# Kernel optimization log

Hardware: AMD Instinct MI355X
Metric: run time of the kernel (lower is better)

The kernel has to match this reference:

```python
import jax, jax.numpy as jnp
import numpy as np

B, N, C = 4, 100000, 64
S = 256            # img_size
RADIUS_PX = 1.5    # radius in pixels
K = 8              # points_per_pixel
GAMMA = 1.0
R_NDC = RADIUS_PX / S * 2.0  # radius in NDC, as in forward()


def setup_inputs() -> dict:
    key = jax.random.key(0)
    k1, k2 = jax.random.split(key)
    pts = jax.random.normal(k1, (B, N, 3), dtype=jnp.float32)
    features = jax.random.normal(k2, (B, N, C), dtype=jnp.float32)
    return {"pts": pts, "features": features}


def _rasterize_one(pts_b):
    # pts_b: (N,3) sign-flipped NDC points. Emulates pytorch3d rasterize_points:
    # per pixel keep the K nearest-in-z points whose NDC distance to the pixel
    # center is <= R_NDC (points with z < 0 are culled).
    x, y, z = pts_b[:, 0], pts_b[:, 1], pts_b[:, 2]
    # pytorch3d NDC->pixel: ndc = 1 - 2*(p+0.5)/S  =>  p = (1-ndc)*S/2 - 0.5
    px = (1.0 - x) * (S / 2.0) - 0.5
    py = (1.0 - y) * (S / 2.0) - 0.5
    offs = jnp.arange(-1, 3)  # 4-wide window fully covers a 1.5px radius
    cj = jnp.floor(px).astype(jnp.int32)[:, None] + offs  # (N,4) candidate cols
    ci = jnp.floor(py).astype(jnp.int32)[:, None] + offs  # (N,4) candidate rows
    cx = 1.0 - 2.0 * (cj.astype(pts_b.dtype) + 0.5) / S   # pixel-center NDC x
    cy = 1.0 - 2.0 * (ci.astype(pts_b.dtype) + 0.5) / S   # pixel-center NDC y
    d2 = (cy - y[:, None])[:, :, None] ** 2 + (cx - x[:, None])[:, None, :] ** 2  # (N,4,4)
    pid = ci[:, :, None] * S + cj[:, None, :]                                      # (N,4,4)
    inb = (ci[:, :, None] >= 0) & (ci[:, :, None] < S) & (cj[:, None, :] >= 0) & (cj[:, None, :] < S)
    valid = inb & (d2 <= R_NDC * R_NDC) & (z[:, None, None] >= 0.0)
    pid = jnp.where(valid, pid, S * S).reshape(-1)
    zc = jnp.where(valid, z[:, None, None], jnp.inf).reshape(-1)
    d2f = d2.reshape(-1)
    pidx = jnp.broadcast_to(jnp.arange(N, dtype=jnp.int32)[:, None, None], (N, 4, 4)).reshape(-1)
    order = jnp.lexsort((zc, pid))  # sort by pixel id, then depth (front first)
    pid_s, d2_s, pi_s = pid[order], d2f[order], pidx[order]
    seg_start = jnp.searchsorted(pid_s, pid_s, side='left')
    rank = jnp.arange(pid_s.shape[0]) - seg_start  # per-pixel z-rank
    keep = (pid_s < S * S) & (rank < K)
    pid_w = jnp.where(keep, pid_s, S * S)          # OOB index -> dropped by mode='drop'
    rank_w = jnp.where(keep, rank, 0)
    idx_buf = jnp.full((S * S, K), -1, jnp.int32).at[pid_w, rank_w].set(pi_s, mode='drop')
    d_buf = jnp.zeros((S * S, K), pts_b.dtype).at[pid_w, rank_w].set(d2_s, mode='drop')
    return idx_buf.reshape(S, S, K), d_buf.reshape(S, S, K)


def _forward(pts, features):
    # forward() flips x and y signs in-place
    pts = pts * jnp.array([-1.0, -1.0, 1.0], dtype=pts.dtype)
    idx, d2 = jax.vmap(_rasterize_one)(pts)        # (B,S,S,K) each
    dist = d2 / (R_NDC * R_NDC)
    alphas = 1.0 - jnp.clip(dist, 0.001, 1.0) ** (0.5 * GAMMA)  # .pow(0.5).pow(gamma)
    alphas = jnp.where(idx >= 0, alphas, 0.0)      # alpha_composite skips idx < 0
    trans = jnp.cumprod(1.0 - alphas, axis=-1)     # transmittance, front-to-back
    trans = jnp.concatenate([jnp.ones_like(trans[..., :1]), trans[..., :-1]], axis=-1)
    w = alphas * trans                             # (B,S,S,K) compositing weights
    gath = jax.vmap(lambda f, i: f[jnp.clip(i, 0)])(features, idx)  # (B,S,S,K,C)
    return jnp.einsum('bhwk,bhwkc->bchw', w, gath)  # (B,C,S,S)


def reference(pts, features):
    return _forward(pts, features)
```

## Files before the change

### kernel.cpp

```cpp
#include <hip/hip_runtime.h>
#include <stdint.h>

#pragma clang fp contract(off)

#define S 256
#define NPTS 100000
#define BATCH 4
#define CCH 64
#define K 8
#define CAP 20

static constexpr float R2 = 0.01171875f * 0.01171875f;
static constexpr unsigned long long SENT = 0xFFFFFFFFFFFFFFFFULL;

__global__ __launch_bounds__(256) void scatter_list_kernel(
        const float* __restrict__ pts,
        unsigned int* __restrict__ counts,
        unsigned long long* __restrict__ lists) {
    int gid = blockIdx.x * blockDim.x + threadIdx.x;
    if (gid >= BATCH * NPTS * 16) return;
    int cell = gid & 15;
    int pid  = gid >> 4;
    int b = pid / NPTS;
    int n = pid - b * NPTS;

    const float* p = pts + (size_t)pid * 3;
    float x = -p[0];
    float y = -p[1];
    float z = p[2];
    if (!(z >= 0.0f)) return;

    float px = (1.0f - x) * 128.0f - 0.5f;
    float py = (1.0f - y) * 128.0f - 0.5f;
    int cj0 = (int)floorf(px);
    int ci0 = (int)floorf(py);

    int ci = ci0 - 1 + (cell >> 2);
    int cj = cj0 - 1 + (cell & 3);
    if (ci < 0 || ci >= S || cj < 0 || cj >= S) return;

    float cy = 1.0f - 2.0f * ((float)ci + 0.5f) / 256.0f;
    float cx = 1.0f - 2.0f * ((float)cj + 0.5f) / 256.0f;
    float dy = cy - y;
    float dx = cx - x;
    float d2 = dy * dy + dx * dx;
    if (!(d2 <= R2)) return;

    unsigned long long key =
        ((unsigned long long)__float_as_uint(z) << 32) | (unsigned int)n;
    size_t base = (size_t)b * (S * S) + (size_t)(ci * S + cj);
    unsigned int old = atomicAdd(&counts[base], 1u);
    if (old < CAP) lists[base * CAP + old] = key;
}

__global__ __launch_bounds__(256) void blend_list_kernel(
        const float* __restrict__ pts,
        const float* __restrict__ feat,
        const unsigned int* __restrict__ counts,
        const unsigned long long* __restrict__ lists,
        float* __restrict__ out) {
    int seg = blockIdx.x;
    int h   = blockIdx.y;
    int b   = blockIdx.z;
    int tid = threadIdx.x;
    int w0  = seg * 64;

    __shared__ float s_alpha[64][K + 1];
    __shared__ float s_wgt[64][K + 1];
    __shared__ int   s_idx[64][K + 1];
    __shared__ int   s_cnt[64];
    __shared__ unsigned long long s_key[64][K];

    const float* pb = pts + (size_t)b * NPTS * 3;

    if (tid < 64) {
        size_t base = (size_t)b * (S * S) + (size_t)h * S + (size_t)(w0 + tid);
        int c = (int)counts[base];
        if (c > CAP) c = CAP;
        const ulonglong2* lp2 =
            reinterpret_cast<const ulonglong2*>(lists + base * (size_t)CAP);
        unsigned long long v[CAP];
#pragma unroll
        for (int j = 0; j < CAP / 2; ++j) {
            unsigned long long lo = SENT, hi = SENT;
            if (2 * j < c) { ulonglong2 t = lp2[j]; lo = t.x; hi = t.y; }
            v[2 * j] = lo;
            v[2 * j + 1] = hi;
        }
#pragma unroll
        for (int j = 0; j < CAP; ++j)
            if (j >= c) v[j] = SENT;
#pragma unroll
        for (int i = 0; i < K; ++i) {
#pragma unroll
            for (int j = i + 1; j < CAP; ++j) {
                unsigned long long a = v[i], q = v[j];
                v[i] = a < q ? a : q;
                v[j] = a < q ? q : a;
            }
        }
#pragma unroll
        for (int k = 0; k < K; ++k) s_key[tid][k] = v[k];
        s_cnt[tid] = c < K ? c : K;
    }
    __syncthreads();

    for (int e = tid; e < 64 * K; e += 256) {
        int p = e >> 3;
        int k = e & 7;
        unsigned long long key = s_key[p][k];
        float alpha = 0.0f;
        int idx = 0;
        if (key != SENT) {
            idx = (int)(unsigned int)(key & 0xFFFFFFFFULL);
            float x = -pb[(size_t)idx * 3 + 0];
            float y = -pb[(size_t)idx * 3 + 1];
            int w = w0 + p;
            float cy = 1.0f - 2.0f * ((float)h + 0.5f) / 256.0f;
            float cx = 1.0f - 2.0f * ((float)w + 0.5f) / 256.0f;
            float dy = cy - y;
            float dx = cx - x;
            float d2 = dy * dy + dx * dx;
            float dist = d2 / R2;
            dist = fminf(fmaxf(dist, 0.001f), 1.0f);
            alpha = 1.0f - sqrtf(dist);
        }
        s_alpha[p][k] = alpha;
        s_idx[p][k] = idx;
    }
    __syncthreads();

    if (tid < 64) {
        float t = 1.0f;
#pragma unroll
        for (int k = 0; k < K; ++k) {
            float a = s_alpha[tid][k];
            s_wgt[tid][k] = a * t;
            t *= (1.0f - a);
        }
    }
    __syncthreads();

    int wave = tid >> 6;
    int lane = tid & 63;
    int pbase = wave * 16;

    int kmax = 0;
#pragma unroll
    for (int i = 0; i < 16; ++i) {
        int c = s_cnt[pbase + i];
        kmax = c > kmax ? c : kmax;
    }

    float acc[16];
#pragma unroll
    for (int i = 0; i < 16; ++i) acc[i] = 0.0f;

    const float* fbl = feat + (size_t)b * NPTS * CCH + lane;
    for (int k = 0; k < kmax; ++k) {
        float v[16];
#pragma unroll
        for (int i = 0; i < 16; ++i) {
            int idx = s_idx[pbase + i][k];
            v[i] = fbl[(size_t)idx << 6];
        }
#pragma unroll
        for (int i = 0; i < 16; ++i) {
            acc[i] += s_wgt[pbase + i][k] * v[i];
        }
    }

    size_t obase = (((size_t)b * CCH + lane) * S + h) * S + (size_t)(w0 + pbase);
    float4* o4 = (float4*)(out + obase);
#pragma unroll
    for (int q = 0; q < 4; ++q) {
        o4[q] = make_float4(acc[4 * q + 0], acc[4 * q + 1],
                            acc[4 * q + 2], acc[4 * q + 3]);
    }
}

__global__ __launch_bounds__(256) void scatter_kernel(
        const float* __restrict__ pts,
        unsigned long long* __restrict__ keys) {
    int gid = blockIdx.x * blockDim.x + threadIdx.x;
    if (gid >= BATCH * NPTS * 16) return;
    int cell = gid & 15;
    int pid  = gid >> 4;
    int b = pid / NPTS;
    int n = pid - b * NPTS;

    const float* p = pts + (size_t)pid * 3;
    float x = -p[0];
    float y = -p[1];
    float z = p[2];
    if (!(z >= 0.0f)) return;

    float px = (1.0f - x) * 128.0f - 0.5f;
    float py = (1.0f - y) * 128.0f - 0.5f;
    int cj0 = (int)floorf(px);
    int ci0 = (int)floorf(py);

    int ci = ci0 - 1 + (cell >> 2);
    int cj = cj0 - 1 + (cell & 3);
    if (ci < 0 || ci >= S || cj < 0 || cj >= S) return;

    float cy = 1.0f - 2.0f * ((float)ci + 0.5f) / 256.0f;
    float cx = 1.0f - 2.0f * ((float)cj + 0.5f) / 256.0f;
    float dy = cy - y;
    float dx = cx - x;
    float d2 = dy * dy + dx * dx;
    if (!(d2 <= R2)) return;

    unsigned long long key =
        ((unsigned long long)__float_as_uint(z) << 32) | (unsigned int)n;
    unsigned long long* slot =
        keys + ((size_t)b * S * S + (size_t)(ci * S + cj)) * K;

    if (slot[K - 1] < key) return;

    for (int s = 0; s < K; ++s) {
        if (key == SENT) break;
        unsigned long long old = atomicMin(&slot[s], key);
        key = old > key ? old : key;
    }
}

__global__ __launch_bounds__(256) void blend_kernel(
        const float* __restrict__ pts,
        const float* __restrict__ feat,
        const unsigned long long* __restrict__ keys,
        float* __restrict__ out) {
    int seg = blockIdx.x;
    int h   = blockIdx.y;
    int b   = blockIdx.z;
    int tid = threadIdx.x;
    int w0  = seg * 64;

    __shared__ float s_alpha[64][K + 1];
    __shared__ float s_wgt[64][K + 1];
    __shared__ int   s_idx[64][K + 1];
    __shared__ int   s_cnt[64];

    const unsigned long long* kb =
        keys + ((size_t)b * S * S + (size_t)h * S + w0) * K;
    const float* pb = pts + (size_t)b * NPTS * 3;

    for (int e = tid; e < 64 * K; e += 256) {
        int p = e >> 3;
        int k = e & 7;
        unsigned long long key = kb[(size_t)p * K + k];
        float alpha = 0.0f;
        int idx = -1;
        if (key != SENT) {
            idx = (int)(unsigned int)(key & 0xFFFFFFFFULL);
            float x = -pb[(size_t)idx * 3 + 0];
            float y = -pb[(size_t)idx * 3 + 1];
            int w = w0 + p;
            float cy = 1.0f - 2.0f * ((float)h + 0.5f) / 256.0f;
            float cx = 1.0f - 2.0f * ((float)w + 0.5f) / 256.0f;
            float dy = cy - y;
            float dx = cx - x;
            float d2 = dy * dy + dx * dx;
            float dist = d2 / R2;
            dist = fminf(fmaxf(dist, 0.001f), 1.0f);
            alpha = 1.0f - sqrtf(dist);
        }
        s_alpha[p][k] = alpha;
        s_idx[p][k] = idx;
    }
    __syncthreads();

    if (tid < 64) {
        float t = 1.0f;
        int cnt = 0;
        for (int k = 0; k < K; ++k) {
            int raw = s_idx[tid][k];
            float a = s_alpha[tid][k];
            s_wgt[tid][k] = a * t;
            t *= (1.0f - a);
            if (raw >= 0) cnt = k + 1;
            s_idx[tid][k] = raw < 0 ? 0 : raw;
        }
        s_cnt[tid] = cnt;
    }
    __syncthreads();

    int wave = tid >> 6;
    int lane = tid & 63;
    int pbase = wave * 16;

    int kmax = 0;
#pragma unroll
    for (int i = 0; i < 16; ++i) {
        int c = s_cnt[pbase + i];
        kmax = c > kmax ? c : kmax;
    }

    float acc[16];
#pragma unroll
    for (int i = 0; i < 16; ++i) acc[i] = 0.0f;

    const float* fbl = feat + (size_t)b * NPTS * CCH + lane;
    for (int k = 0; k < kmax; ++k) {
        float v[16];
#pragma unroll
        for (int i = 0; i < 16; ++i) {
            int idx = s_idx[pbase + i][k];
            v[i] = fbl[(size_t)idx << 6];
        }
#pragma unroll
        for (int i = 0; i < 16; ++i) {
            acc[i] += s_wgt[pbase + i][k] * v[i];
        }
    }

    size_t obase = (((size_t)b * CCH + lane) * S + h) * S + (size_t)(w0 + pbase);
    float4* o4 = (float4*)(out + obase);
#pragma unroll
    for (int q = 0; q < 4; ++q) {
        o4[q] = make_float4(acc[4 * q + 0], acc[4 * q + 1],
                            acc[4 * q + 2], acc[4 * q + 3]);
    }
}

extern "C" void kernel_launch(void* const* d_in, const int* in_sizes, int n_in,
                              void* d_out, int out_size, void* d_ws, size_t ws_size,
                              hipStream_t stream) {
    const float* pts  = (const float*)d_in[0];
    const float* feat = (const float*)d_in[1];
    float* out = (float*)d_out;

    size_t cnt_bytes  = (size_t)BATCH * S * S * sizeof(unsigned int);
    size_t list_bytes = (size_t)BATCH * S * S * CAP * sizeof(unsigned long long);

    if (ws_size >= cnt_bytes + list_bytes) {
        unsigned int* counts = (unsigned int*)d_ws;
        unsigned long long* lists =
            (unsigned long long*)((char*)d_ws + cnt_bytes);
        hipMemsetAsync(counts, 0, cnt_bytes, stream);

        int total = BATCH * NPTS * 16;
        scatter_list_kernel<<<(total + 255) / 256, 256, 0, stream>>>(
            pts, counts, lists);

        dim3 grid(S / 64, S, BATCH);
        blend_list_kernel<<<grid, 256, 0, stream>>>(pts, feat, counts, lists, out);
    } else {
        unsigned long long* keys = (unsigned long long*)d_ws;
        size_t key_bytes = (size_t)BATCH * S * S * K * sizeof(unsigned long long);
        hipMemsetAsync(keys, 0xFF, key_bytes, stream);

        int total = BATCH * NPTS * 16;
        scatter_kernel<<<(total + 255) / 256, 256, 0, stream>>>(pts, keys);

        dim3 grid(S / 64, S, BATCH);
        blend_kernel<<<grid, 256, 0, stream>>>(pts, feat, keys, out);
    }
}
```

Baseline: 242.8 us.

## Swizzle blend blocks across XCDs and use streaming top-8 insertion

The blend kernel moves to a 1D grid of 4096 blocks, remapped so that consecutive logical blocks (same batch, nearby rows) land on the same XCD under round-robin dispatch. This improves L2 locality for the feature gathers of each batch. The fixed 20-element partial selection sort becomes a streaming insertion into eight registers, with a wave-uniform early exit once every lane's list is exhausted, which cuts registers and compare work for sparse pixels. The feature accumulation loop is also unrolled by two.

Result: slower. 248.6 us (+2.4%).

```diff
diff --git a/kernel.cpp b/kernel.cpp
--- a/kernel.cpp
+++ b/kernel.cpp
@@ -53,15 +53,29 @@
     if (old < CAP) lists[base * CAP + old] = key;
 }
 
+#define CSW(a, b) do {                                        \
+        unsigned long long _lo = (a) < (b) ? (a) : (b);       \
+        unsigned long long _hi = (a) < (b) ? (b) : (a);       \
+        (a) = _lo; (b) = _hi;                                 \
+    } while (0)
+#define INSERT8(x) do {                                       \
+        unsigned long long _x = (x);                          \
+        t7 = t7 < _x ? t7 : _x;                               \
+        CSW(t6, t7); CSW(t5, t6); CSW(t4, t5); CSW(t3, t4);   \
+        CSW(t2, t3); CSW(t1, t2); CSW(t0, t1);                \
+    } while (0)
+
 __global__ __launch_bounds__(256) void blend_list_kernel(
         const float* __restrict__ pts,
         const float* __restrict__ feat,
         const unsigned int* __restrict__ counts,
         const unsigned long long* __restrict__ lists,
         float* __restrict__ out) {
-    int seg = blockIdx.x;
-    int h   = blockIdx.y;
-    int b   = blockIdx.z;
+    int blk = blockIdx.x;
+    int logical = (blk & 7) * 512 + (blk >> 3);
+    int seg = logical & 3;
+    int h   = (logical >> 2) & 255;
+    int b   = logical >> 10;
     int tid = threadIdx.x;
     int w0  = seg * 64;
 
@@ -79,28 +93,26 @@
         if (c > CAP) c = CAP;
         const ulonglong2* lp2 =
             reinterpret_cast<const ulonglong2*>(lists + base * (size_t)CAP);
-        unsigned long long v[CAP];
-#pragma unroll
+
+        unsigned long long t0 = SENT, t1 = SENT, t2 = SENT, t3 = SENT;
+        unsigned long long t4 = SENT, t5 = SENT, t6 = SENT, t7 = SENT;
+
         for (int j = 0; j < CAP / 2; ++j) {
+            if (!__any(2 * j < c)) break;
             unsigned long long lo = SENT, hi = SENT;
-            if (2 * j < c) { ulonglong2 t = lp2[j]; lo = t.x; hi = t.y; }
-            v[2 * j] = lo;
-            v[2 * j + 1] = hi;
-        }
-#pragma unroll
-        for (int j = 0; j < CAP; ++j)
-            if (j >= c) v[j] = SENT;
-#pragma unroll
-        for (int i = 0; i < K; ++i) {
-#pragma unroll
-            for (int j = i + 1; j < CAP; ++j) {
-                unsigned long long a = v[i], q = v[j];
-                v[i] = a < q ? a : q;
-                v[j] = a < q ? q : a;
+            if (2 * j < c) {
+                ulonglong2 t = lp2[j];
+                lo = t.x;
+                hi = (2 * j + 1 < c) ? t.y : SENT;
             }
-        }
-#pragma unroll
-        for (int k = 0; k < K; ++k) s_key[tid][k] = v[k];
+            INSERT8(lo);
+            INSERT8(hi);
+        }
+
+        s_key[tid][0] = t0; s_key[tid][1] = t1;
+        s_key[tid][2] = t2; s_key[tid][3] = t3;
+        s_key[tid][4] = t4; s_key[tid][5] = t5;
+        s_key[tid][6] = t6; s_key[tid][7] = t7;
         s_cnt[tid] = c < K ? c : K;
     }
     __syncthreads();
@@ -157,6 +169,7 @@
     for (int i = 0; i < 16; ++i) acc[i] = 0.0f;
 
     const float* fbl = feat + (size_t)b * NPTS * CCH + lane;
+#pragma unroll 2
     for (int k = 0; k < kmax; ++k) {
         float v[16];
 #pragma unroll
@@ -332,6 +345,7 @@
 
     size_t cnt_bytes  = (size_t)BATCH * S * S * sizeof(unsigned int);
     size_t list_bytes = (size_t)BATCH * S * S * CAP * sizeof(unsigned long long);
+    size_t key_bytes  = (size_t)BATCH * S * S * K * sizeof(unsigned long long);
 
     if (ws_size >= cnt_bytes + list_bytes) {
         unsigned int* counts = (unsigned int*)d_ws;
@@ -343,11 +357,9 @@
         scatter_list_kernel<<<(total + 255) / 256, 256, 0, stream>>>(
             pts, counts, lists);
 
-        dim3 grid(S / 64, S, BATCH);
-        blend_list_kernel<<<grid, 256, 0, stream>>>(pts, feat, counts, lists, out);
+        blend_list_kernel<<<4096, 256, 0, stream>>>(pts, feat, counts, lists, out);
     } else {
         unsigned long long* keys = (unsigned long long*)d_ws;
-        size_t key_bytes = (size_t)BATCH * S * S * K * sizeof(unsigned long long);
         hipMemsetAsync(keys, 0xFF, key_bytes, stream);
 
         int total = BATCH * NPTS * 16;
```
